# Optimization experiments

Hardware: AMD Instinct MI355X
Metric: run time of the kernel (lower is better)

## Reference

```python
import jax, jax.numpy as jnp
import numpy as np

D = 1024      # embedding_dim
H = 16        # n_heads
HD = D // H   # head_dim
EPS = 1e-05


def layernorm(x, scale, bias):
    # torch.var default is unbiased (ddof=1) in the original module
    mean = jnp.mean(x, axis=-1, keepdims=True)
    var = jnp.var(x, axis=-1, keepdims=True, ddof=1)
    return scale * (x - mean) / jnp.sqrt(var + EPS) + bias


def gelu(x):
    return 0.5 * x * (1 + jnp.tanh(0.79788456 * (x + 0.044715 * x ** 3)))


def setup_inputs() -> dict:
    key = jax.random.key(0)
    ks = jax.random.split(key, 12)
    s = 0.02
    return {
        "x": jax.random.normal(ks[0], (2, 2048, D), dtype=jnp.float32),
        "Wq": jax.random.normal(ks[1], (D, D), dtype=jnp.float32) * s,
        "Wk": jax.random.normal(ks[2], (D, D), dtype=jnp.float32) * s,
        "Wv": jax.random.normal(ks[3], (D, D), dtype=jnp.float32) * s,
        "Wo": jax.random.normal(ks[4], (D, D), dtype=jnp.float32) * s,
        "bo": jnp.zeros((D,), dtype=jnp.float32),
        "W1": jax.random.normal(ks[5], (D, 4 * D), dtype=jnp.float32) * s,
        "b1": jnp.zeros((4 * D,), dtype=jnp.float32),
        "W2": jax.random.normal(ks[6], (4 * D, D), dtype=jnp.float32) * s,
        "b2": jnp.zeros((D,), dtype=jnp.float32),
        "ln1_scale": jnp.ones((D,), dtype=jnp.float32),
        "ln1_bias": jnp.zeros((D,), dtype=jnp.float32),
        "ln2_scale": jnp.ones((D,), dtype=jnp.float32),
        "ln2_bias": jnp.zeros((D,), dtype=jnp.float32),
    }


def reference(x, Wq, Wk, Wv, Wo, bo, W1, b1, W2, b2,
              ln1_scale, ln1_bias, ln2_scale, ln2_bias):
    B, S, _ = x.shape
    # --- attention sub-block (pre-LN) ---
    h = layernorm(x, ln1_scale, ln1_bias)
    q = (h @ Wq).reshape(B, S, H, HD).transpose(0, 2, 1, 3)  # [B,H,S,HD]
    k = (h @ Wk).reshape(B, S, H, HD).transpose(0, 2, 1, 3)
    v = (h @ Wv).reshape(B, S, H, HD).transpose(0, 2, 1, 3)
    scores = jnp.einsum("bhqd,bhkd->bhqk", q, k)             # [B,H,S,S]
    causal = jnp.tril(jnp.ones((S, S), dtype=bool))
    scores = jnp.where(causal, scores, -jnp.inf)
    attn = jax.nn.softmax(scores / jnp.sqrt(jnp.float32(HD)), axis=-1)
    ctx = jnp.einsum("bhqk,bhkd->bhqd", attn, v)
    ctx = ctx.transpose(0, 2, 1, 3).reshape(B, S, H * HD)
    x = x + (ctx @ Wo + bo)
    # --- FFN sub-block (pre-LN) ---
    h = layernorm(x, ln2_scale, ln2_bias)
    x = x + (gelu(h @ W1 + b1) @ W2 + b2)
    return x
```

## Files before the change

kernel.cpp:

```cpp
#include <hip/hip_runtime.h>
#include <hip/hip_bf16.h>
#include <cstdint>

#define D_DIM 1024
#define S_DIM 2048
#define B_DIM 2
#define NROWS 4096
#define H_DIM 16
#define LOG2E 1.4426950408889634f
#define QSCALE (0.125f * LOG2E)

typedef __bf16 bf16x8 __attribute__((ext_vector_type(8)));
typedef float f32x4 __attribute__((ext_vector_type(4)));
typedef unsigned short u16x8 __attribute__((ext_vector_type(8)));

#define MFMA16(a, b, c) __builtin_amdgcn_mfma_f32_16x16x32_bf16(a, b, c, 0, 0, 0)

__device__ __forceinline__ void async_cp16(const void* g, void* lds) {
  __builtin_amdgcn_global_load_lds(
      (const __attribute__((address_space(1))) void*)(uintptr_t)g,
      (__attribute__((address_space(3))) void*)(uint32_t)(uintptr_t)lds, 16, 0, 0);
}

__device__ __forceinline__ unsigned short f2bf(float f) {
  __hip_bfloat16 h = __float2bfloat16(f);
  return __builtin_bit_cast(unsigned short, h);
}

__device__ __forceinline__ float bf2f(unsigned short u) {
  return __builtin_bit_cast(float, (unsigned int)u << 16);
}

__device__ __forceinline__ float gelu_f(float v) {
  return 0.5f * v * (1.f + tanhf(0.79788456f * (v + 0.044715f * v * v * v)));
}

struct TcArgs {
  const float* src[6];
  __hip_bfloat16* dst[6];
  int K[6];
  int N[6];
  int start[6];
};

__global__ __launch_bounds__(256) void transpose_cast6_kernel(TcArgs a) {
  __shared__ float tile[32][33];
  int bid = blockIdx.x, mi = 0;
#pragma unroll
  for (int i = 1; i < 6; i++)
    if (bid >= a.start[i]) mi = i;
  const float* W = a.src[mi];
  __hip_bfloat16* Wt = a.dst[mi];
  int K = a.K[mi], N = a.N[mi];
  int rel = bid - a.start[mi];
  int tilesx = N >> 5;
  int shift = (N == 4096) ? 7 : 5;
  int n0 = (rel & (tilesx - 1)) * 32, k0 = (rel >> shift) * 32;
  int tx = threadIdx.x, ty = threadIdx.y;
#pragma unroll
  for (int i = 0; i < 32; i += 8)
    tile[ty + i][tx] = W[(size_t)(k0 + ty + i) * N + n0 + tx];
  __syncthreads();
#pragma unroll
  for (int i = 0; i < 32; i += 8)
    Wt[(size_t)(n0 + ty + i) * K + k0 + tx] = __float2bfloat16(tile[tx][ty + i]);
}

__global__ __launch_bounds__(256) void ln_kernel(
    const float* __restrict__ x, const float* __restrict__ sc,
    const float* __restrict__ bi, __hip_bfloat16* __restrict__ out) {
  int row = blockIdx.x, t = threadIdx.x;
  float4 v = ((const float4*)(x + (size_t)row * D_DIM))[t];
  float s = v.x + v.y + v.z + v.w;
  float ss = v.x * v.x + v.y * v.y + v.z * v.z + v.w * v.w;
#pragma unroll
  for (int off = 32; off > 0; off >>= 1) {
    s += __shfl_xor(s, off);
    ss += __shfl_xor(ss, off);
  }
  __shared__ float red[8];
  int wid = t >> 6;
  if ((t & 63) == 0) { red[wid] = s; red[4 + wid] = ss; }
  __syncthreads();
  s = red[0] + red[1] + red[2] + red[3];
  ss = red[4] + red[5] + red[6] + red[7];
  float mean = s * (1.f / 1024.f);
  float var = (ss - 1024.f * mean * mean) * (1.f / 1023.f);
  float inv = rsqrtf(var + 1e-5f);
  float4 scv = ((const float4*)sc)[t];
  float4 biv = ((const float4*)bi)[t];
  ushort4 o;
  o.x = f2bf(scv.x * (v.x - mean) * inv + biv.x);
  o.y = f2bf(scv.y * (v.y - mean) * inv + biv.y);
  o.z = f2bf(scv.z * (v.z - mean) * inv + biv.z);
  o.w = f2bf(scv.w * (v.w - mean) * inv + biv.w);
  ((ushort4*)(out + (size_t)row * D_DIM))[t] = o;
}

template <int BN, int EPI>
__global__ __launch_bounds__(256) void gemm_bt_kernel(
    const __hip_bfloat16* __restrict__ A, const __hip_bfloat16* __restrict__ Bt,
    void* __restrict__ Cout, const float* __restrict__ bias,
    const float* __restrict__ resid, int M, int N, int K, int kchunk) {
  constexpr int NBF = BN / 32;
  __shared__ __hip_bfloat16 As[2][128 * 32];
  __shared__ __hip_bfloat16 Bs[2][BN * 32];
  const int t = threadIdx.x;
  const int lane = t & 63, wid = t >> 6;
  const int ql = lane & 15, g = lane >> 4;
  const int m0 = blockIdx.x * 128, n0 = blockIdx.y * BN;
  const int kz = blockIdx.z;
  const int wm = (wid >> 1) * 64, wn = (wid & 1) * (BN / 2);
  f32x4 acc[4][NBF] = {};
  const int sr = t >> 2, sc8 = (t & 3) * 8;
  const __hip_bfloat16* ag = A + (size_t)(m0 + sr) * K + sc8 + (size_t)kz * kchunk;
  const __hip_bfloat16* bg = Bt + (size_t)(n0 + sr) * K + sc8 + (size_t)kz * kchunk;

  auto stage = [&](int buf, int k0) {
    async_cp16(ag + k0, (char*)&As[buf][0] + wid * 1024);
    async_cp16(ag + (size_t)64 * K + k0, (char*)&As[buf][0] + 4096 + wid * 1024);
    async_cp16(bg + k0, (char*)&Bs[buf][0] + wid * 1024);
    if constexpr (BN == 128)
      async_cp16(bg + (size_t)64 * K + k0, (char*)&Bs[buf][0] + 4096 + wid * 1024);
  };
  auto compute = [&](int buf) {
    bf16x8 af[4], bfr[NBF];
#pragma unroll
    for (int mb = 0; mb < 4; mb++)
      af[mb] = *(const bf16x8*)(&As[buf][(wm + mb * 16 + ql) * 32 + g * 8]);
#pragma unroll
    for (int nb = 0; nb < NBF; nb++)
      bfr[nb] = *(const bf16x8*)(&Bs[buf][(wn + nb * 16 + ql) * 32 + g * 8]);
#pragma unroll
    for (int mb = 0; mb < 4; mb++)
#pragma unroll
      for (int nb = 0; nb < NBF; nb++)
        acc[mb][nb] = MFMA16(af[mb], bfr[nb], acc[mb][nb]);
  };

  stage(0, 0);
  __syncthreads();
  const int nsteps = kchunk >> 5;
  int cur = 0;
  for (int s = 0; s < nsteps - 1; ++s) {
    stage(cur ^ 1, (s + 1) * 32);
    compute(cur);
    __syncthreads();
    cur ^= 1;
  }
  compute(cur);

  const int rb = m0 + wm + (g << 2);
  const int cb = n0 + wn + ql;
#pragma unroll
  for (int mb = 0; mb < 4; mb++) {
#pragma unroll
    for (int nb = 0; nb < NBF; nb++) {
      int col = cb + nb * 16;
#pragma unroll
      for (int r = 0; r < 4; r++) {
        int row = rb + mb * 16 + r;
        float v = acc[mb][nb][r];
        if (EPI == 1) {
          ((float*)Cout)[(size_t)row * N + col] =
              v + bias[col] + resid[(size_t)row * N + col];
        } else if (EPI == 2) {
          ((__hip_bfloat16*)Cout)[(size_t)row * N + col] =
              __float2bfloat16(gelu_f(v + bias[col]));
        } else {
          ((unsigned short*)Cout)[(size_t)kz * ((size_t)M * N) + (size_t)row * N + col] =
              f2bf(v);
        }
      }
    }
  }
}

__global__ __launch_bounds__(256) void ffn2_reduce_kernel(
    const unsigned short* __restrict__ parts, const float* __restrict__ bias,
    const float* __restrict__ resid, float* __restrict__ out) {
  const size_t i = ((size_t)blockIdx.x * 256 + threadIdx.x) * 8;
  const int col = (int)(i & 1023);
  float a[8];
  float4 r0 = *(const float4*)(resid + i);
  float4 r1 = *(const float4*)(resid + i + 4);
  float4 b0 = *(const float4*)(bias + col);
  float4 b1 = *(const float4*)(bias + col + 4);
  a[0] = r0.x + b0.x; a[1] = r0.y + b0.y; a[2] = r0.z + b0.z; a[3] = r0.w + b0.w;
  a[4] = r1.x + b1.x; a[5] = r1.y + b1.y; a[6] = r1.z + b1.z; a[7] = r1.w + b1.w;
#pragma unroll
  for (int c = 0; c < 4; c++) {
    u16x8 p = *(const u16x8*)(parts + (size_t)c * ((size_t)NROWS * 1024) + i);
#pragma unroll
    for (int j = 0; j < 8; j++) a[j] += bf2f(p[j]);
  }
  float4 o0 = {a[0], a[1], a[2], a[3]};
  float4 o1 = {a[4], a[5], a[6], a[7]};
  *(float4*)(out + i) = o0;
  *(float4*)(out + i + 4) = o1;
}

__global__ __launch_bounds__(256) void qkv_kernel(
    const __hip_bfloat16* __restrict__ A, const __hip_bfloat16* __restrict__ Wqt,
    const __hip_bfloat16* __restrict__ Wkt, const __hip_bfloat16* __restrict__ Wvt,
    __hip_bfloat16* __restrict__ qb, __hip_bfloat16* __restrict__ kb,
    unsigned short* __restrict__ vt) {
  __shared__ __hip_bfloat16 As[2][128 * 32];
  __shared__ __hip_bfloat16 Bs[2][128 * 32];
  const int t = threadIdx.x;
  const int lane = t & 63, wid = t >> 6;
  const int ql = lane & 15, g = lane >> 4;
  const int seg = blockIdx.y >> 3;
  const int n0 = (blockIdx.y & 7) * 128;
  const __hip_bfloat16* Bt = seg == 0 ? Wqt : (seg == 1 ? Wkt : Wvt);
  const int m0 = blockIdx.x * 128;
  const int wm = (wid >> 1) * 64, wn = (wid & 1) * 64;
  f32x4 acc[4][4] = {};
  const int sr = t >> 2, sc8 = (t & 3) * 8;
  const __hip_bfloat16* ag = A + (size_t)(m0 + sr) * 1024 + sc8;
  const __hip_bfloat16* bg = Bt + (size_t)(n0 + sr) * 1024 + sc8;

  auto stage = [&](int buf, int k0) {
    async_cp16(ag + k0, (char*)&As[buf][0] + wid * 1024);
    async_cp16(ag + (size_t)64 * 1024 + k0, (char*)&As[buf][0] + 4096 + wid * 1024);
    async_cp16(bg + k0, (char*)&Bs[buf][0] + wid * 1024);
    async_cp16(bg + (size_t)64 * 1024 + k0, (char*)&Bs[buf][0] + 4096 + wid * 1024);
  };
  auto compute = [&](int buf) {
    bf16x8 af[4], bfr[4];
#pragma unroll
    for (int mb = 0; mb < 4; mb++)
      af[mb] = *(const bf16x8*)(&As[buf][(wm + mb * 16 + ql) * 32 + g * 8]);
#pragma unroll
    for (int nb = 0; nb < 4; nb++)
      bfr[nb] = *(const bf16x8*)(&Bs[buf][(wn + nb * 16 + ql) * 32 + g * 8]);
#pragma unroll
    for (int mb = 0; mb < 4; mb++)
#pragma unroll
      for (int nb = 0; nb < 4; nb++)
        acc[mb][nb] = MFMA16(af[mb], bfr[nb], acc[mb][nb]);
  };

  stage(0, 0);
  __syncthreads();
  int cur = 0;
  for (int s = 0; s < 31; ++s) {
    stage(cur ^ 1, (s + 1) * 32);
    compute(cur);
    __syncthreads();
    cur ^= 1;
  }
  compute(cur);

  const int rb = m0 + wm + (g << 2);
  if (seg < 2) {
    __hip_bfloat16* Ob = seg == 0 ? qb : kb;
    const float sc = seg == 0 ? QSCALE : 1.f;
#pragma unroll
    for (int mb = 0; mb < 4; mb++)
#pragma unroll
      for (int nb = 0; nb < 4; nb++) {
        int col = n0 + wn + nb * 16 + ql;
#pragma unroll
        for (int r = 0; r < 4; r++)
          Ob[(size_t)(rb + mb * 16 + r) * 1024 + col] =
              __float2bfloat16(acc[mb][nb][r] * sc);
      }
  } else {
#pragma unroll
    for (int mb = 0; mb < 4; mb++)
#pragma unroll
      for (int nb = 0; nb < 4; nb++) {
        int col = n0 + wn + nb * 16 + ql;
        int h = col >> 6, dh = col & 63;
        int row0 = rb + mb * 16;
        int bb = row0 >> 11, s0 = row0 & 2047;
        ushort4 pk;
        pk.x = f2bf(acc[mb][nb][0]);
        pk.y = f2bf(acc[mb][nb][1]);
        pk.z = f2bf(acc[mb][nb][2]);
        pk.w = f2bf(acc[mb][nb][3]);
        *(ushort4*)(vt + (((size_t)(bb * 16 + h) * 64 + dh) << 11) + s0) = pk;
      }
  }
}

__global__ __launch_bounds__(256) void attn_kernel(
    const __hip_bfloat16* __restrict__ Q, const __hip_bfloat16* __restrict__ Kb,
    const __hip_bfloat16* __restrict__ Vt, __hip_bfloat16* __restrict__ ctx) {
  __shared__ unsigned short Ks[2][64 * 64];
  __shared__ unsigned short Vs[2][64 * 64];
  __shared__ alignas(16) unsigned short Ps[4][16 * 64];
  const int t = threadIdx.x;
  const int lane = t & 63, wid = t >> 6;
  const int ql = lane & 15, g = lane >> 4;
  const int bid = blockIdx.x;
  const int r4 = bid >> 8, k8 = (bid >> 5) & 7, bh = bid & 31;
  const int qt = (r4 == 0) ? 31 - k8 : (r4 == 1) ? 16 + k8 : (r4 == 2) ? 15 - k8 : k8;
  const int b = bh >> 4, hh = bh & 15;
  const int wq0 = qt * 64 + wid * 16;
  const __hip_bfloat16* qp = Q + (size_t)b * S_DIM * D_DIM + hh * 64;
  const __hip_bfloat16* kp = Kb + (size_t)b * S_DIM * D_DIM + hh * 64;
  const __hip_bfloat16* vp = Vt + (size_t)bh * 64 * S_DIM;
  const int kvend = qt * 64 + 64;
  const int swz = (ql & 7) << 4;
  const f32x4 z4 = {0.f, 0.f, 0.f, 0.f};

  auto stageKV = [&](int buf, int kv0) {
    const int sub = lane >> 3, c = lane & 7;
#pragma unroll
    for (int i = 0; i < 2; i++) {
      const int row = wid * 16 + i * 8 + sub;
      const int cs = (c ^ (row & 7)) * 8;
      async_cp16(kp + (size_t)(kv0 + row) * D_DIM + cs,
                 (char*)&Ks[buf][0] + (wid * 16 + i * 8) * 128);
      async_cp16(vp + (size_t)row * S_DIM + kv0 + cs,
                 (char*)&Vs[buf][0] + (wid * 16 + i * 8) * 128);
    }
  };

  bf16x8 qf[2];
#pragma unroll
  for (int hf = 0; hf < 2; hf++)
    qf[hf] = *(const bf16x8*)(qp + (size_t)(wq0 + ql) * D_DIM + hf * 32 + g * 8);

  float m = -3.0e38f, lsum = 0.f;
  f32x4 acc[4] = {};
  unsigned short* Pw = Ps[wid];

  stageKV(0, 0);
  __syncthreads();
  int cur = 0;
  for (int kv0 = 0; kv0 < kvend; kv0 += 64) {
    if (kv0 + 64 < kvend) stageKV(cur ^ 1, kv0 + 64);

    if (kv0 <= wq0 + 15) {
      const char* Kt = (const char*)&Ks[cur][0];
      f32x4 st[4];
#pragma unroll
      for (int ks = 0; ks < 4; ks++) {
        bf16x8 k0 = *(const bf16x8*)(Kt + (ks * 16 + ql) * 128 + ((g * 16) ^ swz));
        bf16x8 k1 = *(const bf16x8*)(Kt + (ks * 16 + ql) * 128 + (((4 + g) * 16) ^ swz));
        st[ks] = MFMA16(k1, qf[1], MFMA16(k0, qf[0], z4));
      }
      if (kv0 + 63 > wq0) {
#pragma unroll
        for (int ks = 0; ks < 4; ks++)
#pragma unroll
          for (int r = 0; r < 4; r++)
            if (kv0 + ks * 16 + 4 * g + r > wq0 + ql) st[ks][r] = -3.0e38f;
      }
      float tm = -3.0e38f;
#pragma unroll
      for (int ks = 0; ks < 4; ks++)
#pragma unroll
        for (int r = 0; r < 4; r++) tm = fmaxf(tm, st[ks][r]);
      tm = fmaxf(tm, __shfl_xor(tm, 16));
      tm = fmaxf(tm, __shfl_xor(tm, 32));
      if (!__all(tm <= m + 8.f)) {
        const float mn = fmaxf(m, tm);
        const float alpha = exp2f(m - mn);
        lsum *= alpha;
#pragma unroll
        for (int db = 0; db < 4; db++) acc[db] *= alpha;
        m = mn;
      }
      float psum = 0.f;
#pragma unroll
      for (int ks = 0; ks < 4; ks++) {
        float p0 = exp2f(st[ks][0] - m), p1 = exp2f(st[ks][1] - m);
        float p2 = exp2f(st[ks][2] - m), p3 = exp2f(st[ks][3] - m);
        psum += (p0 + p1) + (p2 + p3);
        ushort4 pk;
        pk.x = f2bf(p0); pk.y = f2bf(p1); pk.z = f2bf(p2); pk.w = f2bf(p3);
        *(ushort4*)((char*)Pw + ql * 128 + ((ks * 32 + 8 * g) ^ swz)) = pk;
      }
      psum += __shfl_xor(psum, 16);
      psum += __shfl_xor(psum, 32);
      lsum += psum;

      const char* Vtl = (const char*)&Vs[cur][0];
#pragma unroll
      for (int ksl = 0; ksl < 2; ksl++) {
        bf16x8 pb = *(const bf16x8*)((const char*)Pw + ql * 128 + ((ksl * 64 + 16 * g) ^ swz));
#pragma unroll
        for (int db = 0; db < 4; db++) {
          bf16x8 va = *(const bf16x8*)(Vtl + (db * 16 + ql) * 128 + (((ksl * 4 + g) * 16) ^ swz));
          acc[db] = MFMA16(va, pb, acc[db]);
        }
      }
    }
    __syncthreads();
    cur ^= 1;
  }

  const float inv = 1.f / lsum;
  unsigned short* cp = (unsigned short*)ctx + (size_t)(b * S_DIM + wq0 + ql) * D_DIM + hh * 64;
#pragma unroll
  for (int db = 0; db < 4; db++)
#pragma unroll
    for (int i = 0; i < 2; i++) {
      unsigned int lo = f2bf(acc[db][2 * i] * inv);
      unsigned int hi = f2bf(acc[db][2 * i + 1] * inv);
      *(unsigned int*)(cp + db * 16 + 4 * g + 2 * i) = lo | (hi << 16);
    }
}

extern "C" void kernel_launch(void* const* d_in, const int* in_sizes, int n_in,
                              void* d_out, int out_size, void* d_ws, size_t ws_size,
                              hipStream_t stream) {
  const float* x = (const float*)d_in[0];
  const float* Wq = (const float*)d_in[1];
  const float* Wk = (const float*)d_in[2];
  const float* Wv = (const float*)d_in[3];
  const float* Wo = (const float*)d_in[4];
  const float* bo = (const float*)d_in[5];
  const float* W1 = (const float*)d_in[6];
  const float* b1 = (const float*)d_in[7];
  const float* W2 = (const float*)d_in[8];
  const float* b2 = (const float*)d_in[9];
  const float* ln1s = (const float*)d_in[10];
  const float* ln1b = (const float*)d_in[11];
  const float* ln2s = (const float*)d_in[12];
  const float* ln2b = (const float*)d_in[13];
  float* out = (float*)d_out;

  char* p = (char*)d_ws;
  auto take = [&](size_t n) { char* r = p; p += (n + 255) & ~(size_t)255; return r; };
  __hip_bfloat16* Wqt = (__hip_bfloat16*)take((size_t)1024 * 1024 * 2);
  __hip_bfloat16* Wkt = (__hip_bfloat16*)take((size_t)1024 * 1024 * 2);
  __hip_bfloat16* Wvt = (__hip_bfloat16*)take((size_t)1024 * 1024 * 2);
  __hip_bfloat16* Wot = (__hip_bfloat16*)take((size_t)1024 * 1024 * 2);
  __hip_bfloat16* W1t = (__hip_bfloat16*)take((size_t)4096 * 1024 * 2);
  __hip_bfloat16* W2t = (__hip_bfloat16*)take((size_t)4096 * 1024 * 2);
  __hip_bfloat16* hbuf = (__hip_bfloat16*)take((size_t)NROWS * 1024 * 2);
  __hip_bfloat16* qbuf = (__hip_bfloat16*)take((size_t)NROWS * 1024 * 2);
  __hip_bfloat16* kbuf = (__hip_bfloat16*)take((size_t)NROWS * 1024 * 2);
  __hip_bfloat16* vtbuf = (__hip_bfloat16*)take((size_t)NROWS * 1024 * 2);
  __hip_bfloat16* ctxbuf = (__hip_bfloat16*)take((size_t)NROWS * 1024 * 2);
  float* x1buf = (float*)take((size_t)NROWS * 1024 * 4);
  __hip_bfloat16* h2buf = (__hip_bfloat16*)take((size_t)NROWS * 1024 * 2);
  __hip_bfloat16* gbuf = (__hip_bfloat16*)take((size_t)NROWS * 4096 * 2);
  unsigned short* parts = (unsigned short*)hbuf;

  TcArgs ta;
  ta.src[0] = Wq;  ta.dst[0] = Wqt;  ta.K[0] = 1024; ta.N[0] = 1024; ta.start[0] = 0;
  ta.src[1] = Wk;  ta.dst[1] = Wkt;  ta.K[1] = 1024; ta.N[1] = 1024; ta.start[1] = 1024;
  ta.src[2] = Wv;  ta.dst[2] = Wvt;  ta.K[2] = 1024; ta.N[2] = 1024; ta.start[2] = 2048;
  ta.src[3] = Wo;  ta.dst[3] = Wot;  ta.K[3] = 1024; ta.N[3] = 1024; ta.start[3] = 3072;
  ta.src[4] = W1;  ta.dst[4] = W1t;  ta.K[4] = 1024; ta.N[4] = 4096; ta.start[4] = 4096;
  ta.src[5] = W2;  ta.dst[5] = W2t;  ta.K[5] = 4096; ta.N[5] = 1024; ta.start[5] = 8192;
  transpose_cast6_kernel<<<12288, dim3(32, 8), 0, stream>>>(ta);

  ln_kernel<<<NROWS, 256, 0, stream>>>(x, ln1s, ln1b, hbuf);

  qkv_kernel<<<dim3(32, 24), 256, 0, stream>>>(hbuf, Wqt, Wkt, Wvt, qbuf, kbuf,
                                               (unsigned short*)vtbuf);

  attn_kernel<<<1024, 256, 0, stream>>>(qbuf, kbuf, vtbuf, ctxbuf);

  gemm_bt_kernel<64, 1><<<dim3(32, 16, 1), 256, 0, stream>>>(
      ctxbuf, Wot, x1buf, bo, x, NROWS, 1024, 1024, 1024);

  ln_kernel<<<NROWS, 256, 0, stream>>>(x1buf, ln2s, ln2b, h2buf);

  gemm_bt_kernel<128, 2><<<dim3(32, 32, 1), 256, 0, stream>>>(
      h2buf, W1t, gbuf, b1, nullptr, NROWS, 4096, 1024, 1024);

  gemm_bt_kernel<128, 3><<<dim3(32, 8, 4), 256, 0, stream>>>(
      gbuf, W2t, parts, nullptr, nullptr, NROWS, 1024, 4096, 1024);

  ffn2_reduce_kernel<<<2048, 256, 0, stream>>>(parts, b2, x1buf, out);
}
```

Baseline: 245.5 us.

## Replace QKV and FFN GEMMs with a hand-scheduled 256x256 tile kernel

Adds a 512-thread GEMM kernel with 256x256 output tiles and an XOR-swizzled 128KB LDS double buffer. It uses explicit waitcnt, barrier and sched_barrier placement and raises wave priority around the MFMA groups. This one kernel now runs the QKV projection (treating Wq/Wk/Wv as one contiguous 3072-wide matrix), FFN1 with a GELU epilogue, and the split-K FFN2. The goal is more data reuse per tile and better overlap of loads with MFMA work. The GELU is rewritten as the equivalent sigmoid form using exp2 and a fast reciprocal. The larger tiles give fewer blocks (192–256), so some CUs can sit idle, and the QKV path depends on the transposed weights being adjacent in memory.

```diff
diff --git a/kernel.cpp b/kernel.cpp
--- a/kernel.cpp
+++ b/kernel.cpp
@@ -15,6 +15,11 @@
 typedef unsigned short u16x8 __attribute__((ext_vector_type(8)));
 
 #define MFMA16(a, b, c) __builtin_amdgcn_mfma_f32_16x16x32_bf16(a, b, c, 0, 0, 0)
+#define SBAR __builtin_amdgcn_sched_barrier(0)
+#define WBAR __builtin_amdgcn_s_barrier()
+#define LGKM0 { asm volatile("s_waitcnt lgkmcnt(0)" ::: "memory"); SBAR; }
+#define VM6 { asm volatile("s_waitcnt vmcnt(6)" ::: "memory"); SBAR; }
+#define VM0 { asm volatile("s_waitcnt vmcnt(0)" ::: "memory"); SBAR; }
 
 __device__ __forceinline__ void async_cp16(const void* g, void* lds) {
   __builtin_amdgcn_global_load_lds(
@@ -31,8 +36,11 @@
   return __builtin_bit_cast(float, (unsigned int)u << 16);
 }
 
-__device__ __forceinline__ float gelu_f(float v) {
-  return 0.5f * v * (1.f + tanhf(0.79788456f * (v + 0.044715f * v * v * v)));
+__device__ __forceinline__ float gelu_fast(float v) {
+  float u = v * v;
+  float w = v * fmaf(u, 0.044715f, 1.f);
+  float e = exp2f(w * -2.3022161f);
+  return v * __builtin_amdgcn_rcpf(1.f + e);
 }
 
 struct TcArgs {
@@ -95,6 +103,160 @@
   o.z = f2bf(scv.z * (v.z - mean) * inv + biv.z);
   o.w = f2bf(scv.w * (v.w - mean) * inv + biv.w);
   ((ushort4*)(out + (size_t)row * D_DIM))[t] = o;
+}
+
+template <int EPI>
+__global__ __launch_bounds__(512) void gemm256_kernel(
+    const __hip_bfloat16* __restrict__ A, const __hip_bfloat16* __restrict__ Bt,
+    void* __restrict__ Cout, const float* __restrict__ bias,
+    __hip_bfloat16* __restrict__ qb, __hip_bfloat16* __restrict__ kb,
+    unsigned short* __restrict__ vt, int strideA, int strideB) {
+  __shared__ char lds[131072];
+  const int t = threadIdx.x;
+  const int lane = t & 63, wid = t >> 6;
+  const int ql = lane & 15, g = lane >> 4;
+  const int wr = wid >> 2, wc = wid & 3;
+  const int m0 = blockIdx.x * 256, n0 = blockIdx.y * 256;
+  const int koff = blockIdx.z * 1024;
+  const int sw = (ql & 7) << 4;
+
+  const int srow = t >> 3;
+  const int scol = ((t & 7) << 4) ^ ((srow & 7) << 4);
+  const __hip_bfloat16* aBase = A + (size_t)(m0 + srow) * strideA + koff + (scol >> 1);
+  const __hip_bfloat16* bBase = Bt + (size_t)(n0 + srow) * strideB + koff + (scol >> 1);
+  const uint32_t ldsT = (uint32_t)(t * 16);
+
+  auto stgA = [&](int kt, int half) {
+    char* dst = lds + ((kt & 1) * 2 + half) * 16384 + ldsT;
+    const __hip_bfloat16* src = aBase + (size_t)(half * 128) * strideA + kt * 64;
+    async_cp16(src, dst);
+    async_cp16(src + (size_t)64 * strideA, dst + 8192);
+  };
+  auto stgB = [&](int kt, int half) {
+    char* dst = lds + 65536 + ((kt & 1) * 2 + half) * 16384 + ldsT;
+    const __hip_bfloat16* src = bBase + (size_t)(half * 128) * strideB + kt * 64;
+    async_cp16(src, dst);
+    async_cp16(src + (size_t)64 * strideB, dst + 8192);
+  };
+
+  bf16x8 aR[4][2], bR[2][2][2];
+  f32x4 acc[8][4] = {};
+
+  auto ldA = [&](int slot, int mh) {
+    const char* base = lds + (slot * 2 + wr) * 16384;
+#pragma unroll
+    for (int mi = 0; mi < 4; mi++)
+#pragma unroll
+      for (int kk = 0; kk < 2; kk++)
+        aR[mi][kk] = *(const bf16x8*)(base + (mh * 64 + mi * 16 + ql) * 128 +
+                                      ((kk * 64 + g * 16) ^ sw));
+  };
+  auto ldB = [&](int slot, int nh) {
+    const char* base = lds + 65536 + (slot * 2 + (wc >> 1)) * 16384;
+#pragma unroll
+    for (int ni = 0; ni < 2; ni++)
+#pragma unroll
+      for (int kk = 0; kk < 2; kk++)
+        bR[nh][ni][kk] = *(const bf16x8*)(base + ((wc & 1) * 64 + nh * 32 + ni * 16 + ql) * 128 +
+                                          ((kk * 64 + g * 16) ^ sw));
+  };
+  auto mma = [&](int mh, int nh) {
+    __builtin_amdgcn_s_setprio(1);
+#pragma unroll
+    for (int mi = 0; mi < 4; mi++)
+#pragma unroll
+      for (int ni = 0; ni < 2; ni++) {
+        f32x4 c = acc[mh * 4 + mi][nh * 2 + ni];
+        c = MFMA16(aR[mi][0], bR[nh][ni][0], c);
+        c = MFMA16(aR[mi][1], bR[nh][ni][1], c);
+        acc[mh * 4 + mi][nh * 2 + ni] = c;
+      }
+    __builtin_amdgcn_s_setprio(0);
+  };
+
+  stgB(0, 0); stgA(0, 0); stgB(0, 1); stgA(0, 1);
+  stgB(1, 0); stgB(1, 1); stgA(1, 0);
+  VM6; WBAR;
+
+#pragma unroll 1
+  for (int i = 0; i < 7; i++) {
+    const int k2 = 2 * i;
+    ldA(0, 0); ldB(0, 0); stgA(k2 + 1, 1); SBAR; WBAR; LGKM0; mma(0, 0); WBAR;
+    ldB(0, 1); stgB(k2 + 2, 0); SBAR; WBAR; LGKM0; mma(0, 1); WBAR;
+    ldA(0, 1); stgB(k2 + 2, 1); SBAR; WBAR; LGKM0; mma(1, 1); WBAR;
+    stgA(k2 + 2, 0); SBAR; WBAR; LGKM0; mma(1, 0); VM6; WBAR;
+    ldA(1, 0); ldB(1, 0); stgA(k2 + 2, 1); SBAR; WBAR; LGKM0; mma(0, 0); WBAR;
+    ldB(1, 1); stgB(k2 + 3, 0); SBAR; WBAR; LGKM0; mma(0, 1); WBAR;
+    ldA(1, 1); stgB(k2 + 3, 1); SBAR; WBAR; LGKM0; mma(1, 1); WBAR;
+    stgA(k2 + 3, 0); SBAR; WBAR; LGKM0; mma(1, 0); VM6; WBAR;
+  }
+  ldA(0, 0); ldB(0, 0); stgA(15, 1); SBAR; WBAR; LGKM0; mma(0, 0); WBAR;
+  ldB(0, 1); SBAR; WBAR; LGKM0; mma(0, 1); WBAR;
+  ldA(0, 1); SBAR; WBAR; LGKM0; mma(1, 1); WBAR;
+  SBAR; WBAR; LGKM0; mma(1, 0); VM0; WBAR;
+  ldA(1, 0); ldB(1, 0); SBAR; WBAR; LGKM0; mma(0, 0); WBAR;
+  ldB(1, 1); SBAR; WBAR; LGKM0; mma(0, 1); WBAR;
+  ldA(1, 1); SBAR; WBAR; LGKM0; mma(1, 1); WBAR;
+  mma(1, 0);
+
+  const int rb = m0 + wr * 128 + (g << 2);
+  const int cb = wc * 64 + ql;
+  if (EPI == 0) {
+    const int seg = n0 >> 10;
+    if (seg < 2) {
+      __hip_bfloat16* Ob = seg == 0 ? qb : kb;
+      const float sc = seg == 0 ? QSCALE : 1.f;
+#pragma unroll
+      for (int mb = 0; mb < 8; mb++)
+#pragma unroll
+        for (int nb = 0; nb < 4; nb++) {
+          int col = (n0 & 1023) + cb + nb * 16;
+#pragma unroll
+          for (int rr = 0; rr < 4; rr++)
+            Ob[(size_t)(rb + mb * 16 + rr) * 1024 + col] =
+                __float2bfloat16(acc[mb][nb][rr] * sc);
+        }
+    } else {
+#pragma unroll
+      for (int mb = 0; mb < 8; mb++)
+#pragma unroll
+        for (int nb = 0; nb < 4; nb++) {
+          int csub = (n0 & 1023) + cb + nb * 16;
+          int h = csub >> 6, dh = csub & 63;
+          int row0 = rb + mb * 16;
+          int bb = row0 >> 11, s0 = row0 & 2047;
+          ushort4 pk;
+          pk.x = f2bf(acc[mb][nb][0]);
+          pk.y = f2bf(acc[mb][nb][1]);
+          pk.z = f2bf(acc[mb][nb][2]);
+          pk.w = f2bf(acc[mb][nb][3]);
+          *(ushort4*)(vt + (((size_t)(bb * 16 + h) * 64 + dh) << 11) + s0) = pk;
+        }
+    }
+  } else if (EPI == 1) {
+#pragma unroll
+    for (int mb = 0; mb < 8; mb++)
+#pragma unroll
+      for (int nb = 0; nb < 4; nb++) {
+        int col = n0 + cb + nb * 16;
+        float bv = bias[col];
+#pragma unroll
+        for (int rr = 0; rr < 4; rr++)
+          ((__hip_bfloat16*)Cout)[(size_t)(rb + mb * 16 + rr) * 4096 + col] =
+              __float2bfloat16(gelu_fast(acc[mb][nb][rr] + bv));
+      }
+  } else {
+    unsigned short* Cp = (unsigned short*)Cout + (size_t)blockIdx.z * NROWS * 1024;
+#pragma unroll
+    for (int mb = 0; mb < 8; mb++)
+#pragma unroll
+      for (int nb = 0; nb < 4; nb++) {
+        int col = n0 + cb + nb * 16;
+#pragma unroll
+        for (int rr = 0; rr < 4; rr++)
+          Cp[(size_t)(rb + mb * 16 + rr) * 1024 + col] = f2bf(acc[mb][nb][rr]);
+      }
+  }
 }
 
 template <int BN, int EPI>
@@ -164,12 +326,6 @@
         if (EPI == 1) {
           ((float*)Cout)[(size_t)row * N + col] =
               v + bias[col] + resid[(size_t)row * N + col];
-        } else if (EPI == 2) {
-          ((__hip_bfloat16*)Cout)[(size_t)row * N + col] =
-              __float2bfloat16(gelu_f(v + bias[col]));
-        } else {
-          ((unsigned short*)Cout)[(size_t)kz * ((size_t)M * N) + (size_t)row * N + col] =
-              f2bf(v);
         }
       }
     }
@@ -198,91 +354,6 @@
   float4 o1 = {a[4], a[5], a[6], a[7]};
   *(float4*)(out + i) = o0;
   *(float4*)(out + i + 4) = o1;
-}
-
-__global__ __launch_bounds__(256) void qkv_kernel(
-    const __hip_bfloat16* __restrict__ A, const __hip_bfloat16* __restrict__ Wqt,
-    const __hip_bfloat16* __restrict__ Wkt, const __hip_bfloat16* __restrict__ Wvt,
-    __hip_bfloat16* __restrict__ qb, __hip_bfloat16* __restrict__ kb,
-    unsigned short* __restrict__ vt) {
-  __shared__ __hip_bfloat16 As[2][128 * 32];
-  __shared__ __hip_bfloat16 Bs[2][128 * 32];
-  const int t = threadIdx.x;
-  const int lane = t & 63, wid = t >> 6;
-  const int ql = lane & 15, g = lane >> 4;
-  const int seg = blockIdx.y >> 3;
-  const int n0 = (blockIdx.y & 7) * 128;
-  const __hip_bfloat16* Bt = seg == 0 ? Wqt : (seg == 1 ? Wkt : Wvt);
-  const int m0 = blockIdx.x * 128;
-  const int wm = (wid >> 1) * 64, wn = (wid & 1) * 64;
-  f32x4 acc[4][4] = {};
-  const int sr = t >> 2, sc8 = (t & 3) * 8;
-  const __hip_bfloat16* ag = A + (size_t)(m0 + sr) * 1024 + sc8;
-  const __hip_bfloat16* bg = Bt + (size_t)(n0 + sr) * 1024 + sc8;
-
-  auto stage = [&](int buf, int k0) {
-    async_cp16(ag + k0, (char*)&As[buf][0] + wid * 1024);
-    async_cp16(ag + (size_t)64 * 1024 + k0, (char*)&As[buf][0] + 4096 + wid * 1024);
-    async_cp16(bg + k0, (char*)&Bs[buf][0] + wid * 1024);
-    async_cp16(bg + (size_t)64 * 1024 + k0, (char*)&Bs[buf][0] + 4096 + wid * 1024);
-  };
-  auto compute = [&](int buf) {
-    bf16x8 af[4], bfr[4];
-#pragma unroll
-    for (int mb = 0; mb < 4; mb++)
-      af[mb] = *(const bf16x8*)(&As[buf][(wm + mb * 16 + ql) * 32 + g * 8]);
-#pragma unroll
-    for (int nb = 0; nb < 4; nb++)
-      bfr[nb] = *(const bf16x8*)(&Bs[buf][(wn + nb * 16 + ql) * 32 + g * 8]);
-#pragma unroll
-    for (int mb = 0; mb < 4; mb++)
-#pragma unroll
-      for (int nb = 0; nb < 4; nb++)
-        acc[mb][nb] = MFMA16(af[mb], bfr[nb], acc[mb][nb]);
-  };
-
-  stage(0, 0);
-  __syncthreads();
-  int cur = 0;
-  for (int s = 0; s < 31; ++s) {
-    stage(cur ^ 1, (s + 1) * 32);
-    compute(cur);
-    __syncthreads();
-    cur ^= 1;
-  }
-  compute(cur);
-
-  const int rb = m0 + wm + (g << 2);
-  if (seg < 2) {
-    __hip_bfloat16* Ob = seg == 0 ? qb : kb;
-    const float sc = seg == 0 ? QSCALE : 1.f;
-#pragma unroll
-    for (int mb = 0; mb < 4; mb++)
-#pragma unroll
-      for (int nb = 0; nb < 4; nb++) {
-        int col = n0 + wn + nb * 16 + ql;
-#pragma unroll
-        for (int r = 0; r < 4; r++)
-          Ob[(size_t)(rb + mb * 16 + r) * 1024 + col] =
-              __float2bfloat16(acc[mb][nb][r] * sc);
-      }
-  } else {
-#pragma unroll
-    for (int mb = 0; mb < 4; mb++)
-#pragma unroll
-      for (int nb = 0; nb < 4; nb++) {
-        int col = n0 + wn + nb * 16 + ql;
-        int h = col >> 6, dh = col & 63;
-        int row0 = rb + mb * 16;
-        int bb = row0 >> 11, s0 = row0 & 2047;
-        ushort4 pk;
-        pk.x = f2bf(acc[mb][nb][0]);
-        pk.y = f2bf(acc[mb][nb][1]);
-        pk.z = f2bf(acc[mb][nb][2]);
-        pk.w = f2bf(acc[mb][nb][3]);
-        *(ushort4*)(vt + (((size_t)(bb * 16 + h) * 64 + dh) << 11) + s0) = pk;
-      }
-  }
 }
 
 __global__ __launch_bounds__(256) void attn_kernel(
@@ -454,8 +525,8 @@
 
   ln_kernel<<<NROWS, 256, 0, stream>>>(x, ln1s, ln1b, hbuf);
 
-  qkv_kernel<<<dim3(32, 24), 256, 0, stream>>>(hbuf, Wqt, Wkt, Wvt, qbuf, kbuf,
-                                               (unsigned short*)vtbuf);
+  gemm256_kernel<0><<<dim3(16, 12), 512, 0, stream>>>(
+      hbuf, Wqt, nullptr, nullptr, qbuf, kbuf, (unsigned short*)vtbuf, 1024, 1024);
 
   attn_kernel<<<1024, 256, 0, stream>>>(qbuf, kbuf, vtbuf, ctxbuf);
 
@@ -464,11 +535,11 @@
 
   ln_kernel<<<NROWS, 256, 0, stream>>>(x1buf, ln2s, ln2b, h2buf);
 
-  gemm_bt_kernel<128, 2><<<dim3(32, 32, 1), 256, 0, stream>>>(
-      h2buf, W1t, gbuf, b1, nullptr, NROWS, 4096, 1024, 1024);
-
-  gemm_bt_kernel<128, 3><<<dim3(32, 8, 4), 256, 0, stream>>>(
-      gbuf, W2t, parts, nullptr, nullptr, NROWS, 1024, 4096, 1024);
+  gemm256_kernel<1><<<dim3(16, 16), 512, 0, stream>>>(
+      h2buf, W1t, gbuf, b1, nullptr, nullptr, nullptr, 1024, 1024);
+
+  gemm256_kernel<2><<<dim3(16, 4, 4), 512, 0, stream>>>(
+      gbuf, W2t, parts, nullptr, nullptr, nullptr, nullptr, 4096, 4096);
 
   ffn2_reduce_kernel<<<2048, 256, 0, stream>>>(parts, b2, x1buf, out);
 }
```

Measured after the change: 205.8 us. 1.19x faster.

## Unify GEMMs with XCD-aware block swizzle and a cheaper exp2-based GELU

Applied to the files above, without the earlier changes.

Folds the separate QKV kernel into one generic 128x128 GEMM template whose epilogue is chosen by a template parameter. It remaps block indices so consecutive blocks on each of the 8 XCDs share A/B tiles, aiming for better L2 reuse. The attention output projection moves from 64-wide to 128-wide N tiles, giving fewer, larger blocks. GELU now uses an exp2 and reciprocal sigmoid form instead of tanhf to shorten the FFN1 epilogue. The fused QKV path relies on the Wq, Wk and Wv transposes sitting contiguously in memory, and the swizzle assumes the block count is a multiple of 8.

```diff
diff --git a/kernel.cpp b/kernel.cpp
--- a/kernel.cpp
+++ b/kernel.cpp
@@ -31,8 +31,11 @@
   return __builtin_bit_cast(float, (unsigned int)u << 16);
 }
 
-__device__ __forceinline__ float gelu_f(float v) {
-  return 0.5f * v * (1.f + tanhf(0.79788456f * (v + 0.044715f * v * v * v)));
+__device__ __forceinline__ float gelu_fast(float v) {
+  float u = v * v;
+  float w = v * fmaf(u, 0.044715f, 1.f);
+  float e = exp2f(w * -2.3022161f);
+  return v * __builtin_amdgcn_rcpf(1.f + e);
 }
 
 struct TcArgs {
@@ -97,21 +100,27 @@
   ((ushort4*)(out + (size_t)row * D_DIM))[t] = o;
 }
 
-template <int BN, int EPI>
+template <int EPI>
 __global__ __launch_bounds__(256) void gemm_bt_kernel(
     const __hip_bfloat16* __restrict__ A, const __hip_bfloat16* __restrict__ Bt,
     void* __restrict__ Cout, const float* __restrict__ bias,
-    const float* __restrict__ resid, int M, int N, int K, int kchunk) {
-  constexpr int NBF = BN / 32;
+    const float* __restrict__ resid, __hip_bfloat16* __restrict__ qb,
+    __hip_bfloat16* __restrict__ kb, unsigned short* __restrict__ vt,
+    int K, int kchunk) {
   __shared__ __hip_bfloat16 As[2][128 * 32];
-  __shared__ __hip_bfloat16 Bs[2][BN * 32];
+  __shared__ __hip_bfloat16 Bs[2][128 * 32];
   const int t = threadIdx.x;
   const int lane = t & 63, wid = t >> 6;
   const int ql = lane & 15, g = lane >> 4;
-  const int m0 = blockIdx.x * 128, n0 = blockIdx.y * BN;
+  const int nbx = gridDim.x;
+  const int nwg = nbx * gridDim.y;
+  const int lin = blockIdx.y * nbx + blockIdx.x;
+  const int cpx = nwg >> 3;
+  const int u = (lin & 7) * cpx + (lin >> 3);
+  const int m0 = (u % nbx) * 128, n0 = (u / nbx) * 128;
   const int kz = blockIdx.z;
-  const int wm = (wid >> 1) * 64, wn = (wid & 1) * (BN / 2);
-  f32x4 acc[4][NBF] = {};
+  const int wm = (wid >> 1) * 64, wn = (wid & 1) * 64;
+  f32x4 acc[4][4] = {};
   const int sr = t >> 2, sc8 = (t & 3) * 8;
   const __hip_bfloat16* ag = A + (size_t)(m0 + sr) * K + sc8 + (size_t)kz * kchunk;
   const __hip_bfloat16* bg = Bt + (size_t)(n0 + sr) * K + sc8 + (size_t)kz * kchunk;
@@ -120,21 +129,20 @@
     async_cp16(ag + k0, (char*)&As[buf][0] + wid * 1024);
     async_cp16(ag + (size_t)64 * K + k0, (char*)&As[buf][0] + 4096 + wid * 1024);
     async_cp16(bg + k0, (char*)&Bs[buf][0] + wid * 1024);
-    if constexpr (BN == 128)
-      async_cp16(bg + (size_t)64 * K + k0, (char*)&Bs[buf][0] + 4096 + wid * 1024);
+    async_cp16(bg + (size_t)64 * K + k0, (char*)&Bs[buf][0] + 4096 + wid * 1024);
   };
   auto compute = [&](int buf) {
-    bf16x8 af[4], bfr[NBF];
+    bf16x8 af[4], bfr[4];
 #pragma unroll
     for (int mb = 0; mb < 4; mb++)
       af[mb] = *(const bf16x8*)(&As[buf][(wm + mb * 16 + ql) * 32 + g * 8]);
 #pragma unroll
-    for (int nb = 0; nb < NBF; nb++)
+    for (int nb = 0; nb < 4; nb++)
       bfr[nb] = *(const bf16x8*)(&Bs[buf][(wn + nb * 16 + ql) * 32 + g * 8]);
 #pragma unroll
     for (int mb = 0; mb < 4; mb++)
 #pragma unroll
-      for (int nb = 0; nb < NBF; nb++)
+      for (int nb = 0; nb < 4; nb++)
         acc[mb][nb] = MFMA16(af[mb], bfr[nb], acc[mb][nb]);
   };
 
@@ -151,26 +159,46 @@
   compute(cur);
 
   const int rb = m0 + wm + (g << 2);
-  const int cb = n0 + wn + ql;
 #pragma unroll
   for (int mb = 0; mb < 4; mb++) {
 #pragma unroll
-    for (int nb = 0; nb < NBF; nb++) {
-      int col = cb + nb * 16;
-#pragma unroll
-      for (int r = 0; r < 4; r++) {
-        int row = rb + mb * 16 + r;
-        float v = acc[mb][nb][r];
-        if (EPI == 1) {
-          ((float*)Cout)[(size_t)row * N + col] =
-              v + bias[col] + resid[(size_t)row * N + col];
-        } else if (EPI == 2) {
-          ((__hip_bfloat16*)Cout)[(size_t)row * N + col] =
-              __float2bfloat16(gelu_f(v + bias[col]));
+    for (int nb = 0; nb < 4; nb++) {
+      const int col = n0 + wn + nb * 16 + ql;
+      const f32x4 c = acc[mb][nb];
+      const int row0 = rb + mb * 16;
+      if (EPI == 0) {
+        const int seg = col >> 10;
+        const int c1k = col & 1023;
+        if (seg < 2) {
+          __hip_bfloat16* Ob = seg == 0 ? qb : kb;
+          const float sc = seg == 0 ? QSCALE : 1.f;
+#pragma unroll
+          for (int rr = 0; rr < 4; rr++)
+            Ob[(size_t)(row0 + rr) * 1024 + c1k] = __float2bfloat16(c[rr] * sc);
         } else {
-          ((unsigned short*)Cout)[(size_t)kz * ((size_t)M * N) + (size_t)row * N + col] =
-              f2bf(v);
+          const int h = c1k >> 6, dh = c1k & 63;
+          const int bb = row0 >> 11, s0 = row0 & 2047;
+          ushort4 pk;
+          pk.x = f2bf(c[0]); pk.y = f2bf(c[1]); pk.z = f2bf(c[2]); pk.w = f2bf(c[3]);
+          *(ushort4*)(vt + (((size_t)(bb * 16 + h) * 64 + dh) << 11) + s0) = pk;
         }
+      } else if (EPI == 1) {
+        const float bv = bias[col];
+#pragma unroll
+        for (int rr = 0; rr < 4; rr++)
+          ((float*)Cout)[(size_t)(row0 + rr) * 1024 + col] =
+              c[rr] + bv + resid[(size_t)(row0 + rr) * 1024 + col];
+      } else if (EPI == 2) {
+        const float bv = bias[col];
+#pragma unroll
+        for (int rr = 0; rr < 4; rr++)
+          ((__hip_bfloat16*)Cout)[(size_t)(row0 + rr) * 4096 + col] =
+              __float2bfloat16(gelu_fast(c[rr] + bv));
+      } else {
+        unsigned short* Cp = (unsigned short*)Cout + (size_t)kz * NROWS * 1024;
+#pragma unroll
+        for (int rr = 0; rr < 4; rr++)
+          Cp[(size_t)(row0 + rr) * 1024 + col] = f2bf(c[rr]);
       }
     }
   }
@@ -198,91 +226,6 @@
   float4 o1 = {a[4], a[5], a[6], a[7]};
   *(float4*)(out + i) = o0;
   *(float4*)(out + i + 4) = o1;
-}
-
-__global__ __launch_bounds__(256) void qkv_kernel(
-    const __hip_bfloat16* __restrict__ A, const __hip_bfloat16* __restrict__ Wqt,
-    const __hip_bfloat16* __restrict__ Wkt, const __hip_bfloat16* __restrict__ Wvt,
-    __hip_bfloat16* __restrict__ qb, __hip_bfloat16* __restrict__ kb,
-    unsigned short* __restrict__ vt) {
-  __shared__ __hip_bfloat16 As[2][128 * 32];
-  __shared__ __hip_bfloat16 Bs[2][128 * 32];
-  const int t = threadIdx.x;
-  const int lane = t & 63, wid = t >> 6;
-  const int ql = lane & 15, g = lane >> 4;
-  const int seg = blockIdx.y >> 3;
-  const int n0 = (blockIdx.y & 7) * 128;
-  const __hip_bfloat16* Bt = seg == 0 ? Wqt : (seg == 1 ? Wkt : Wvt);
-  const int m0 = blockIdx.x * 128;
-  const int wm = (wid >> 1) * 64, wn = (wid & 1) * 64;
-  f32x4 acc[4][4] = {};
-  const int sr = t >> 2, sc8 = (t & 3) * 8;
-  const __hip_bfloat16* ag = A + (size_t)(m0 + sr) * 1024 + sc8;
-  const __hip_bfloat16* bg = Bt + (size_t)(n0 + sr) * 1024 + sc8;
-
-  auto stage = [&](int buf, int k0) {
-    async_cp16(ag + k0, (char*)&As[buf][0] + wid * 1024);
-    async_cp16(ag + (size_t)64 * 1024 + k0, (char*)&As[buf][0] + 4096 + wid * 1024);
-    async_cp16(bg + k0, (char*)&Bs[buf][0] + wid * 1024);
-    async_cp16(bg + (size_t)64 * 1024 + k0, (char*)&Bs[buf][0] + 4096 + wid * 1024);
-  };
-  auto compute = [&](int buf) {
-    bf16x8 af[4], bfr[4];
-#pragma unroll
-    for (int mb = 0; mb < 4; mb++)
-      af[mb] = *(const bf16x8*)(&As[buf][(wm + mb * 16 + ql) * 32 + g * 8]);
-#pragma unroll
-    for (int nb = 0; nb < 4; nb++)
-      bfr[nb] = *(const bf16x8*)(&Bs[buf][(wn + nb * 16 + ql) * 32 + g * 8]);
-#pragma unroll
-    for (int mb = 0; mb < 4; mb++)
-#pragma unroll
-      for (int nb = 0; nb < 4; nb++)
-        acc[mb][nb] = MFMA16(af[mb], bfr[nb], acc[mb][nb]);
-  };
-
-  stage(0, 0);
-  __syncthreads();
-  int cur = 0;
-  for (int s = 0; s < 31; ++s) {
-    stage(cur ^ 1, (s + 1) * 32);
-    compute(cur);
-    __syncthreads();
-    cur ^= 1;
-  }
-  compute(cur);
-
-  const int rb = m0 + wm + (g << 2);
-  if (seg < 2) {
-    __hip_bfloat16* Ob = seg == 0 ? qb : kb;
-    const float sc = seg == 0 ? QSCALE : 1.f;
-#pragma unroll
-    for (int mb = 0; mb < 4; mb++)
-#pragma unroll
-      for (int nb = 0; nb < 4; nb++) {
-        int col = n0 + wn + nb * 16 + ql;
-#pragma unroll
-        for (int r = 0; r < 4; r++)
-          Ob[(size_t)(rb + mb * 16 + r) * 1024 + col] =
-              __float2bfloat16(acc[mb][nb][r] * sc);
-      }
-  } else {
-#pragma unroll
-    for (int mb = 0; mb < 4; mb++)
-#pragma unroll
-      for (int nb = 0; nb < 4; nb++) {
-        int col = n0 + wn + nb * 16 + ql;
-        int h = col >> 6, dh = col & 63;
-        int row0 = rb + mb * 16;
-        int bb = row0 >> 11, s0 = row0 & 2047;
-        ushort4 pk;
-        pk.x = f2bf(acc[mb][nb][0]);
-        pk.y = f2bf(acc[mb][nb][1]);
-        pk.z = f2bf(acc[mb][nb][2]);
-        pk.w = f2bf(acc[mb][nb][3]);
-        *(ushort4*)(vt + (((size_t)(bb * 16 + h) * 64 + dh) << 11) + s0) = pk;
-      }
-  }
 }
 
 __global__ __launch_bounds__(256) void attn_kernel(
@@ -454,21 +397,22 @@
 
   ln_kernel<<<NROWS, 256, 0, stream>>>(x, ln1s, ln1b, hbuf);
 
-  qkv_kernel<<<dim3(32, 24), 256, 0, stream>>>(hbuf, Wqt, Wkt, Wvt, qbuf, kbuf,
-                                               (unsigned short*)vtbuf);
+  gemm_bt_kernel<0><<<dim3(32, 24), 256, 0, stream>>>(
+      hbuf, Wqt, nullptr, nullptr, nullptr, qbuf, kbuf, (unsigned short*)vtbuf,
+      1024, 1024);
 
   attn_kernel<<<1024, 256, 0, stream>>>(qbuf, kbuf, vtbuf, ctxbuf);
 
-  gemm_bt_kernel<64, 1><<<dim3(32, 16, 1), 256, 0, stream>>>(
-      ctxbuf, Wot, x1buf, bo, x, NROWS, 1024, 1024, 1024);
+  gemm_bt_kernel<1><<<dim3(32, 8), 256, 0, stream>>>(
+      ctxbuf, Wot, x1buf, bo, x, nullptr, nullptr, nullptr, 1024, 1024);
 
   ln_kernel<<<NROWS, 256, 0, stream>>>(x1buf, ln2s, ln2b, h2buf);
 
-  gemm_bt_kernel<128, 2><<<dim3(32, 32, 1), 256, 0, stream>>>(
-      h2buf, W1t, gbuf, b1, nullptr, NROWS, 4096, 1024, 1024);
-
-  gemm_bt_kernel<128, 3><<<dim3(32, 8, 4), 256, 0, stream>>>(
-      gbuf, W2t, parts, nullptr, nullptr, NROWS, 1024, 4096, 1024);
+  gemm_bt_kernel<2><<<dim3(32, 32), 256, 0, stream>>>(
+      h2buf, W1t, gbuf, b1, nullptr, nullptr, nullptr, nullptr, 1024, 1024);
+
+  gemm_bt_kernel<3><<<dim3(32, 8, 4), 256, 0, stream>>>(
+      gbuf, W2t, parts, nullptr, nullptr, nullptr, nullptr, nullptr, 4096, 1024);
 
   ffn2_reduce_kernel<<<2048, 256, 0, stream>>>(parts, b2, x1buf, out);
 }
```

Result: slower. 255.9 us (+4.2%).
